# Performance work log

Hardware: AMD Instinct MI355X
Metric: run time of the kernel (lower is better)

## Reference

```python
import jax, jax.numpy as jnp
import numpy as np

B, C_IN, N_IN, N_OUT = 4, 64, 8192, 8192
D1, F, H = 4, 15, 16384  # d+1, filter_size, max_hash_cnt
C_MID, C_OUT = 64, 64
LEAK = 0.01


def setup_inputs() -> dict:
    key = jax.random.key(0)
    ks = jax.random.split(key, 10)
    features = jax.random.normal(ks[0], (B, C_IN, N_IN), jnp.float32)
    in_barycentric = jax.random.uniform(ks[1], (B, D1, N_IN), dtype=jnp.float32)
    # global flat lattice offsets: local vertex id in [0,H) plus per-batch base b*(H+1)
    local_off = jax.random.randint(ks[2], (B, D1, N_IN), 0, H)
    base = (jnp.arange(B, dtype=jnp.int64) * (H + 1))[:, None, None]
    in_lattice_offset = local_off.astype(jnp.int64) + base
    # neighbor ids in [-1, H); -1 means missing -> maps to zero padding slot after +1
    blur_neighbors = (jax.random.randint(ks[3], (B, F, H), 0, H + 1) - 1).astype(jnp.int64)
    out_barycentric = jax.random.uniform(ks[4], (B, D1, N_OUT), dtype=jnp.float32)
    out_lattice_offset = jax.random.randint(ks[5], (B, D1, N_OUT), 0, H).astype(jnp.int64)
    # blur conv params: layer0 Conv2d(C_IN,C_MID,(F,1)) + LeakyReLU, layer1 Conv2d(C_MID,C_OUT,(1,1)) no relu
    W0 = jax.random.normal(ks[6], (C_MID, C_IN, F), jnp.float32) * 0.05
    b0 = jax.random.normal(ks[7], (C_MID,), jnp.float32) * 0.01
    W1 = jax.random.normal(ks[8], (C_OUT, C_MID), jnp.float32) * 0.1
    b1 = jax.random.normal(ks[9], (C_OUT,), jnp.float32) * 0.01
    bias = jnp.zeros((C_OUT,), jnp.float32)  # slice bias, initialized to zeros as in module
    return dict(features=features, in_barycentric=in_barycentric,
                in_lattice_offset=in_lattice_offset, blur_neighbors=blur_neighbors,
                out_barycentric=out_barycentric, out_lattice_offset=out_lattice_offset,
                W0=W0, b0=b0, W1=W1, b1=b1, bias=bias)


def reference(features, in_barycentric, in_lattice_offset, blur_neighbors,
              out_barycentric, out_lattice_offset, W0, b0, W1, b1, bias):
    b_sz, c_in, n_in = features.shape
    max_hash = blur_neighbors.shape[-1]
    # ---- splat: scatter-sum barycentric-weighted features onto lattice vertices ----
    vals = in_barycentric[:, None, :, :] * features[:, :, None, :]      # (B,C,d1,N)
    vals = vals.transpose(0, 2, 3, 1).reshape(-1, c_in)                  # (B*d1*N, C)
    idx = (in_lattice_offset + 1).reshape(-1)                            # (B*d1*N,)
    splat = jax.ops.segment_sum(vals, idx, num_segments=b_sz * (max_hash + 1))
    splat = splat.reshape(b_sz, max_hash + 1, c_in).transpose(0, 2, 1)   # (B,C,H+1)
    # normalization: splat of all-ones feature
    one_splat = jax.ops.segment_sum(in_barycentric.reshape(-1), idx,
                                    num_segments=b_sz * (max_hash + 1))
    one_splat = one_splat.reshape(b_sz, max_hash + 1)
    splat = splat / (one_splat + 1e-5)[:, None, :]
    # ---- blur: gather F neighbors per vertex, then conv over the filter axis ----
    spread = jax.vmap(lambda s, n: s[:, n])(splat, blur_neighbors + 1)   # (B,C,F,H)
    h0 = jnp.einsum('bcfh,ocf->boh', spread, W0) + b0[None, :, None]     # (B,C_mid,H)
    h0 = jnp.where(h0 > 0, h0, LEAK * h0)                                # LeakyReLU
    feat_blurred = jnp.einsum('boh,po->bph', h0, W1) + b1[None, :, None] # (B,C_out,H)
    # ---- slice: barycentric-weighted gather back to output points ----
    tmp = jax.vmap(lambda f, o: f[:, o])(feat_blurred, out_lattice_offset)  # (B,C_out,d1,N_out)
    sliced = (out_barycentric[:, None, :, :] * tmp).sum(axis=2)
    sliced = sliced + bias[None, :, None]
    return sliced
```

## Files before the change

### kernel.cpp

```cpp
#include <hip/hip_runtime.h>

#define NB 4
#define C_IN 64
#define N_IN 8192
#define N_OUT 8192
#define D1 4
#define FS 15
#define HSZ 16384
#define LEAK 0.01f
#define CAP 24
#define POISON 0xAAAAAAAAu

#define NVERT (NB*(HSZ+1))

typedef __attribute__((ext_vector_type(8))) short short8;
typedef __attribute__((ext_vector_type(4))) float floatx4;

#define SPLATB_OFF 0
#define SPLATB_FL  (NVERT*32)
#define W0B_OFF    (SPLATB_OFF + SPLATB_FL)
#define W0B_FL     (64*64*FS/2)
#define W1B_OFF    (W0B_OFF + W0B_FL)
#define W1B_FL     (64*64/2)
#define CNT_OFF    (W1B_OFF + W1B_FL)
#define CNT_FL     (NVERT)
#define BREG_OFF   (CNT_OFF + CNT_FL)
#define FEATB_OFF  (BREG_OFF)
#define FEATB_FL   (NB*N_IN*32)
#define ENTID_OFF  (FEATB_OFF + FEATB_FL)
#define ENT_FL     (NVERT*CAP)
#define ENTW_OFF   (ENTID_OFF + ENT_FL)
#define FB_OFF     (BREG_OFF)

__device__ inline ushort f2bf(float x) {
    uint u = __float_as_uint(x);
    return (ushort)((u + 0x7FFF + ((u >> 16) & 1)) >> 16);
}
__device__ inline float bf2f(ushort b) {
    return __uint_as_float(((uint)b) << 16);
}

__global__ __launch_bounds__(256) void prep(const float* __restrict__ feat,
                                            const float* __restrict__ W0,
                                            const float* __restrict__ W1,
                                            const int* __restrict__ off,
                                            const float* __restrict__ bary,
                                            ushort* __restrict__ featB,
                                            ushort* __restrict__ W0f,
                                            ushort* __restrict__ W1f,
                                            uint* __restrict__ cnt,
                                            int* __restrict__ ent_id,
                                            float* __restrict__ ent_w) {
    __shared__ float t[64 * 65];
    const int blk = blockIdx.x;
    const int tid = threadIdx.x;
    if (blk < 512) {
        const int b  = blk >> 7;
        const int nb = (blk & 127) << 6;
        const int l  = tid & 63;
        const int g  = tid >> 6;
#pragma unroll
        for (int i = 0; i < 16; ++i) {
            int c = g * 16 + i;
            t[c * 65 + l] = feat[((size_t)(b * 64 + c)) * N_IN + nb + l];
        }
        __syncthreads();
#pragma unroll
        for (int i = 0; i < 16; ++i) {
            int n = g * 16 + i;
            featB[((size_t)(b * N_IN) + nb + n) * 64 + l] = f2bf(t[l * 65 + n]);
        }
    } else if (blk < 1024) {
        int e = (blk - 512) * 256 + tid;
        int v = off[e] + 1;
        int n = e & (N_IN - 1);
        int b = e >> 15;
        uint old  = atomicAdd(&cnt[v], 1u);
        uint slot = (old >= POISON) ? (old - POISON) : old;
        if (slot < CAP) {
            ent_id[v * CAP + slot] = b * N_IN + n;
            ent_w [v * CAP + slot] = bary[e];
        }
    } else {
        int e = (blk - 1024) * 256 + tid;
        if (e < 64 * 64 * FS) {
            int j    = e & 7;
            int lane = (e >> 3) & 63;
            int ch   = (e >> 9) & 1;
            int ot   = (e >> 10) & 3;
            int f    = e >> 12;
            int o = ot * 16 + (lane & 15);
            int c = ch * 32 + ((lane >> 4) & 3) * 8 + j;
            W0f[e] = f2bf(W0[(o * 64 + c) * FS + f]);
        } else {
            int e2   = e - 64 * 64 * FS;
            int j    = e2 & 7;
            int lane = (e2 >> 3) & 63;
            int ch   = (e2 >> 9) & 1;
            int pt   = (e2 >> 10) & 3;
            int p = pt * 16 + (lane & 15);
            int o = ch * 32 + ((lane >> 4) & 3) * 8 + j;
            W1f[e2] = f2bf(W1[p * 64 + o]);
        }
    }
}

__global__ __launch_bounds__(256) void gather_splat(const ushort* __restrict__ featB,
                                                    uint* __restrict__ cnt,
                                                    const int* __restrict__ ent_id,
                                                    const float* __restrict__ ent_w,
                                                    ushort* __restrict__ splatB) {
    const int v    = blockIdx.x * 4 + (threadIdx.x >> 6);
    const int lane = threadIdx.x & 63;
    uint cv = cnt[v];
    if (lane == 0) cnt[v] = 0u;
    int c = (int)((cv >= POISON) ? (cv - POISON) : cv);
    if (c > CAP) c = CAP;
    float acc = 0.f, sw = 0.f;
    const int base = v * CAP;
    for (int e0 = 0; e0 < c; e0 += 4) {
        const int kn = c - e0;
        int   id[4];
        float wt[4];
#pragma unroll
        for (int k = 0; k < 4; ++k) {
            id[k] = ent_id[base + e0 + k];
            wt[k] = ent_w [base + e0 + k];
        }
        float fv[4];
#pragma unroll
        for (int k = 0; k < 4; ++k)
            if (k < kn) fv[k] = bf2f(featB[(size_t)id[k] * 64 + lane]);
#pragma unroll
        for (int k = 0; k < 4; ++k)
            if (k < kn) { acc += wt[k] * fv[k]; sw += wt[k]; }
    }
    splatB[(size_t)v * 64 + lane] = f2bf(acc / (sw + 1e-5f));
}

#define XSTR 72
__global__ __launch_bounds__(256, 4) void blur_mfma(const ushort* __restrict__ splatB,
                                                    const int* __restrict__ nbr,
                                                    const ushort* __restrict__ W0f,
                                                    const ushort* __restrict__ W1f,
                                                    const float* __restrict__ b0,
                                                    const float* __restrict__ b1,
                                                    ushort* __restrict__ fb) {
    __shared__ ushort Xs[2][64 * XSTR];

    const int tid = threadIdx.x;
    const int p   = blockIdx.x;
    const int b   = p & 3;
    const int hb  = (p >> 2) << 6;

    const int lane = tid & 63;
    const int w    = tid >> 6;
    const int ow   = w & 1;
    const int hw   = w >> 1;
    const int m    = lane & 15;
    const int q    = lane >> 4;

    const int r    = tid >> 2;
    const int sseg = (tid & 3) << 4;

    const int* nbase = nbr + (b * FS) * HSZ + hb;
    const size_t sbase = (size_t)b * (HSZ + 1) * 64;

    short8 acur[2][2], anxt[2][2];
#pragma unroll
    for (int ot = 0; ot < 2; ++ot)
#pragma unroll
        for (int ch = 0; ch < 2; ++ch)
            acur[ot][ch] = *(const short8*)&W0f[(((ow * 2 + ot) * 2 + ch) * 64 + lane) * 8];

    {
        int v = nbase[r] + 1;
        const ushort* row = splatB + sbase + (size_t)v * 64 + sseg;
        *(short8*)&Xs[0][r * XSTR + sseg]     = *(const short8*)&row[0];
        *(short8*)&Xs[0][r * XSTR + sseg + 8] = *(const short8*)&row[8];
    }
    int nv = nbase[HSZ + r] + 1;
    __syncthreads();

    floatx4 acc[2][2] = {};

    for (int f = 0; f < FS; ++f) {
        const int cur = f & 1, nxt = cur ^ 1;
        short8 px0, px1;
        int nn = 0;
        if (f < FS - 1) {
            const ushort* row = splatB + sbase + (size_t)nv * 64 + sseg;
            px0 = *(const short8*)&row[0];
            px1 = *(const short8*)&row[8];
#pragma unroll
            for (int ot = 0; ot < 2; ++ot)
#pragma unroll
                for (int ch = 0; ch < 2; ++ch)
                    anxt[ot][ch] = *(const short8*)
                        &W0f[((((f + 1) * 4 + ow * 2 + ot) * 2 + ch) * 64 + lane) * 8];
            if (f < FS - 2) nn = nbase[(f + 2) * HSZ + r] + 1;
        }
#pragma unroll
        for (int ch = 0; ch < 2; ++ch) {
            const int ko = ch * 32 + q * 8;
#pragma unroll
            for (int ht = 0; ht < 2; ++ht) {
                short8 bb = *(const short8*)&Xs[cur][(hw * 32 + ht * 16 + m) * XSTR + ko];
                acc[0][ht] = __builtin_amdgcn_mfma_f32_16x16x32_bf16(acur[0][ch], bb, acc[0][ht], 0, 0, 0);
                acc[1][ht] = __builtin_amdgcn_mfma_f32_16x16x32_bf16(acur[1][ch], bb, acc[1][ht], 0, 0, 0);
            }
        }
        if (f < FS - 1) {
            *(short8*)&Xs[nxt][r * XSTR + sseg]     = px0;
            *(short8*)&Xs[nxt][r * XSTR + sseg + 8] = px1;
            nv = nn;
#pragma unroll
            for (int ot = 0; ot < 2; ++ot)
#pragma unroll
                for (int ch = 0; ch < 2; ++ch)
                    acur[ot][ch] = anxt[ot][ch];
        }
        __syncthreads();
    }

    short8 a2[2][2];
#pragma unroll
    for (int pt = 0; pt < 2; ++pt)
#pragma unroll
        for (int ch = 0; ch < 2; ++ch)
            a2[pt][ch] = *(const short8*)&W1f[(((ow * 2 + pt) * 2 + ch) * 64 + lane) * 8];

    ushort* Hs = &Xs[0][0];
#pragma unroll
    for (int ot = 0; ot < 2; ++ot) {
        const float4 b0v = *(const float4*)(b0 + ow * 32 + ot * 16 + q * 4);
#pragma unroll
        for (int ht = 0; ht < 2; ++ht) {
            float v0 = acc[ot][ht][0] + b0v.x; v0 = v0 > 0.f ? v0 : LEAK * v0;
            float v1 = acc[ot][ht][1] + b0v.y; v1 = v1 > 0.f ? v1 : LEAK * v1;
            float v2 = acc[ot][ht][2] + b0v.z; v2 = v2 > 0.f ? v2 : LEAK * v2;
            float v3 = acc[ot][ht][3] + b0v.w; v3 = v3 > 0.f ? v3 : LEAK * v3;
            ushort4 hv;
            hv.x = f2bf(v0); hv.y = f2bf(v1); hv.z = f2bf(v2); hv.w = f2bf(v3);
            *(ushort4*)&Hs[(hw * 32 + ht * 16 + m) * XSTR + ow * 32 + ot * 16 + q * 4] = hv;
        }
    }
    __syncthreads();

    floatx4 acc2[2][2] = {};
#pragma unroll
    for (int ch = 0; ch < 2; ++ch) {
        const int ko = ch * 32 + q * 8;
#pragma unroll
        for (int ht = 0; ht < 2; ++ht) {
            short8 b2 = *(const short8*)&Hs[(hw * 32 + ht * 16 + m) * XSTR + ko];
            acc2[0][ht] = __builtin_amdgcn_mfma_f32_16x16x32_bf16(a2[0][ch], b2, acc2[0][ht], 0, 0, 0);
            acc2[1][ht] = __builtin_amdgcn_mfma_f32_16x16x32_bf16(a2[1][ch], b2, acc2[1][ht], 0, 0, 0);
        }
    }

#pragma unroll
    for (int pt = 0; pt < 2; ++pt) {
        const float4 b1v = *(const float4*)(b1 + ow * 32 + pt * 16 + q * 4);
#pragma unroll
        for (int ht = 0; ht < 2; ++ht) {
            ushort4 ov;
            ov.x = f2bf(acc2[pt][ht][0] + b1v.x);
            ov.y = f2bf(acc2[pt][ht][1] + b1v.y);
            ov.z = f2bf(acc2[pt][ht][2] + b1v.z);
            ov.w = f2bf(acc2[pt][ht][3] + b1v.w);
            *(ushort4*)&fb[((size_t)(b * HSZ) + hb + hw * 32 + ht * 16 + m) * 64
                           + ow * 32 + pt * 16 + q * 4] = ov;
        }
    }
}

__global__ __launch_bounds__(256) void slice_kernel(const ushort* __restrict__ fb,
                                                    const float* __restrict__ ob,
                                                    const int* __restrict__ off,
                                                    const float* __restrict__ bias,
                                                    float* __restrict__ out) {
    __shared__ float tile[64 * 17];
    const int blk  = blockIdx.x;
    const int b    = blk & 3;
    const int nb   = (blk >> 2) << 4;
    const int lane = threadIdx.x & 63;
    const int w    = threadIdx.x >> 6;

    const float bs = bias[lane];
#pragma unroll
    for (int t = 0; t < 4; ++t) {
        int nl = w * 4 + t;
        int n  = nb + nl;
        float acc = bs;
#pragma unroll
        for (int j = 0; j < D1; ++j) {
            float wj = ob[(b * D1 + j) * N_OUT + n];
            int   oj = off[(b * D1 + j) * N_OUT + n];
            acc += wj * bf2f(fb[((size_t)b * HSZ + oj) * 64 + lane]);
        }
        tile[lane * 17 + nl] = acc;
    }
    __syncthreads();
    {
        const int p  = threadIdx.x >> 2;
        const int c4 = (threadIdx.x & 3) << 2;
        float4 v;
        v.x = tile[p * 17 + c4 + 0];
        v.y = tile[p * 17 + c4 + 1];
        v.z = tile[p * 17 + c4 + 2];
        v.w = tile[p * 17 + c4 + 3];
        *(float4*)&out[((size_t)(b * 64 + p)) * N_OUT + nb + c4] = v;
    }
}

extern "C" void kernel_launch(void* const* d_in, const int* in_sizes, int n_in,
                              void* d_out, int out_size, void* d_ws, size_t ws_size,
                              hipStream_t stream) {
    const float* features = (const float*)d_in[0];
    const float* in_bary  = (const float*)d_in[1];
    const int*   in_off   = (const int*)d_in[2];
    const int*   nbr      = (const int*)d_in[3];
    const float* out_bary = (const float*)d_in[4];
    const int*   out_off  = (const int*)d_in[5];
    const float* W0       = (const float*)d_in[6];
    const float* b0       = (const float*)d_in[7];
    const float* W1       = (const float*)d_in[8];
    const float* b1       = (const float*)d_in[9];
    const float* bias     = (const float*)d_in[10];

    float*  ws     = (float*)d_ws;
    ushort* splatB = (ushort*)(ws + SPLATB_OFF);
    ushort* W0f    = (ushort*)(ws + W0B_OFF);
    ushort* W1f    = (ushort*)(ws + W1B_OFF);
    uint*   cnt    = (uint*)(ws + CNT_OFF);
    ushort* featB  = (ushort*)(ws + FEATB_OFF);
    int*    ent_id = (int*)(ws + ENTID_OFF);
    float*  ent_w  = ws + ENTW_OFF;
    ushort* fb     = (ushort*)(ws + FB_OFF);


    prep<<<1280, 256, 0, stream>>>(features, W0, W1, in_off, in_bary,
                                   featB, W0f, W1f, cnt, ent_id, ent_w);
    gather_splat<<<NVERT / 4, 256, 0, stream>>>(featB, cnt, ent_id, ent_w, splatB);
    blur_mfma<<<NB * (HSZ / 64), 256, 0, stream>>>(splatB, nbr, W0f, W1f, b0, b1, fb);
    slice_kernel<<<NB * (N_OUT / 16), 256, 0, stream>>>(fb, out_bary, out_off, bias, (float*)d_out);
}
```

Baseline: 137.4 us.

## Fuse splat, blur and slice stages into one cooperative persistent kernel

Result: slower. 406.3 us (+195.8%).

```diff
diff --git a/kernel.cpp b/kernel.cpp
--- a/kernel.cpp
+++ b/kernel.cpp
@@ -1,4 +1,7 @@
 #include <hip/hip_runtime.h>
+#include <hip/hip_cooperative_groups.h>
+
+namespace cg = cooperative_groups;
 
 #define NB 4
 #define C_IN 64
@@ -32,12 +35,286 @@
 #define ENTW_OFF   (ENTID_OFF + ENT_FL)
 #define FB_OFF     (BREG_OFF)
 
+#define XSTR 72
+
 __device__ inline ushort f2bf(float x) {
     uint u = __float_as_uint(x);
     return (ushort)((u + 0x7FFF + ((u >> 16) & 1)) >> 16);
 }
 __device__ inline float bf2f(ushort b) {
     return __uint_as_float(((uint)b) << 16);
+}
+
+__global__ __launch_bounds__(256, 4) void fused_all(
+    const float* __restrict__ feat, const float* __restrict__ bary,
+    const int* __restrict__ in_off, const int* __restrict__ nbr,
+    const float* __restrict__ ob,   const int* __restrict__ out_off,
+    const float* __restrict__ W0,   const float* __restrict__ b0,
+    const float* __restrict__ W1,   const float* __restrict__ b1,
+    const float* __restrict__ bias,
+    ushort* __restrict__ featB, ushort* __restrict__ W0f, ushort* __restrict__ W1f,
+    uint* cnt, int* __restrict__ ent_id, float* __restrict__ ent_w,
+    ushort* __restrict__ splatB, ushort* __restrict__ fb, float* __restrict__ out)
+{
+    cg::grid_group grid = cg::this_grid();
+    __shared__ __align__(16) ushort sm[2 * 64 * XSTR];
+    const int tid = threadIdx.x;
+    const int nbk = gridDim.x;
+
+    for (int blk = blockIdx.x; blk < 1280; blk += nbk) {
+        if (blk < 512) {
+            float* t = (float*)sm;
+            const int b  = blk >> 7;
+            const int nb = (blk & 127) << 6;
+            const int l  = tid & 63;
+            const int g  = tid >> 6;
+#pragma unroll
+            for (int i = 0; i < 16; ++i) {
+                int c = g * 16 + i;
+                t[c * 65 + l] = feat[((size_t)(b * 64 + c)) * N_IN + nb + l];
+            }
+            __syncthreads();
+#pragma unroll
+            for (int i = 0; i < 16; ++i) {
+                int n = g * 16 + i;
+                featB[((size_t)(b * N_IN) + nb + n) * 64 + l] = f2bf(t[l * 65 + n]);
+            }
+            __syncthreads();
+        } else if (blk < 1024) {
+            int e = (blk - 512) * 256 + tid;
+            int v = in_off[e] + 1;
+            int n = e & (N_IN - 1);
+            int b = e >> 15;
+            uint old  = atomicAdd(&cnt[v], 1u);
+            uint slot = (old >= POISON) ? (old - POISON) : old;
+            if (slot < CAP) {
+                ent_id[v * CAP + slot] = b * N_IN + n;
+                ent_w [v * CAP + slot] = bary[e];
+            }
+        } else {
+            int e = (blk - 1024) * 256 + tid;
+            if (e < 64 * 64 * FS) {
+                int j    = e & 7;
+                int lane = (e >> 3) & 63;
+                int ch   = (e >> 9) & 1;
+                int ot   = (e >> 10) & 3;
+                int f    = e >> 12;
+                int o = ot * 16 + (lane & 15);
+                int c = ch * 32 + ((lane >> 4) & 3) * 8 + j;
+                W0f[e] = f2bf(W0[(o * 64 + c) * FS + f]);
+            } else {
+                int e2   = e - 64 * 64 * FS;
+                int j    = e2 & 7;
+                int lane = (e2 >> 3) & 63;
+                int ch   = (e2 >> 9) & 1;
+                int pt   = (e2 >> 10) & 3;
+                int p = pt * 16 + (lane & 15);
+                int o = ch * 32 + ((lane >> 4) & 3) * 8 + j;
+                W1f[e2] = f2bf(W1[p * 64 + o]);
+            }
+        }
+    }
+    grid.sync();
+
+    {
+        const int lane = tid & 63;
+        for (int vb = blockIdx.x; vb < NVERT / 4; vb += nbk) {
+            const int v = vb * 4 + (tid >> 6);
+            uint cv = cnt[v];
+            if (lane == 0) cnt[v] = 0u;
+            int c = (int)((cv >= POISON) ? (cv - POISON) : cv);
+            if (c > CAP) c = CAP;
+            float acc = 0.f, sw = 0.f;
+            const int base = v * CAP;
+            for (int e0 = 0; e0 < c; e0 += 4) {
+                const int kn = c - e0;
+                int   id[4];
+                float wt[4];
+#pragma unroll
+                for (int k = 0; k < 4; ++k) {
+                    id[k] = ent_id[base + e0 + k];
+                    wt[k] = ent_w [base + e0 + k];
+                }
+                float fv[4];
+#pragma unroll
+                for (int k = 0; k < 4; ++k)
+                    if (k < kn) fv[k] = bf2f(featB[(size_t)id[k] * 64 + lane]);
+#pragma unroll
+                for (int k = 0; k < 4; ++k)
+                    if (k < kn) { acc += wt[k] * fv[k]; sw += wt[k]; }
+            }
+            splatB[(size_t)v * 64 + lane] = f2bf(acc / (sw + 1e-5f));
+        }
+    }
+    grid.sync();
+
+    for (int p = blockIdx.x; p < NB * (HSZ / 64); p += nbk) {
+        ushort* Xs0 = sm;
+        ushort* Xs1 = sm + 64 * XSTR;
+
+        const int b   = p & 3;
+        const int hb  = (p >> 2) << 6;
+
+        const int lane = tid & 63;
+        const int w    = tid >> 6;
+        const int ow   = w & 1;
+        const int hw   = w >> 1;
+        const int m    = lane & 15;
+        const int q    = lane >> 4;
+
+        const int r    = tid >> 2;
+        const int sseg = (tid & 3) << 4;
+
+        const int* nbase = nbr + (b * FS) * HSZ + hb;
+        const size_t sbase = (size_t)b * (HSZ + 1) * 64;
+
+        short8 acur[2][2], anxt[2][2];
+#pragma unroll
+        for (int ot = 0; ot < 2; ++ot)
+#pragma unroll
+            for (int ch = 0; ch < 2; ++ch)
+                acur[ot][ch] = *(const short8*)&W0f[(((ow * 2 + ot) * 2 + ch) * 64 + lane) * 8];
+
+        {
+            int v = nbase[r] + 1;
+            const ushort* row = splatB + sbase + (size_t)v * 64 + sseg;
+            *(short8*)&Xs0[r * XSTR + sseg]     = *(const short8*)&row[0];
+            *(short8*)&Xs0[r * XSTR + sseg + 8] = *(const short8*)&row[8];
+        }
+        int nv = nbase[HSZ + r] + 1;
+        __syncthreads();
+
+        floatx4 acc[2][2] = {};
+
+        for (int f = 0; f < FS; ++f) {
+            ushort* Xc = (f & 1) ? Xs1 : Xs0;
+            ushort* Xn = (f & 1) ? Xs0 : Xs1;
+            short8 px0, px1;
+            int nn = 0;
+            if (f < FS - 1) {
+                const ushort* row = splatB + sbase + (size_t)nv * 64 + sseg;
+                px0 = *(const short8*)&row[0];
+                px1 = *(const short8*)&row[8];
+#pragma unroll
+                for (int ot = 0; ot < 2; ++ot)
+#pragma unroll
+                    for (int ch = 0; ch < 2; ++ch)
+                        anxt[ot][ch] = *(const short8*)
+                            &W0f[((((f + 1) * 4 + ow * 2 + ot) * 2 + ch) * 64 + lane) * 8];
+                if (f < FS - 2) nn = nbase[(f + 2) * HSZ + r] + 1;
+            }
+#pragma unroll
+            for (int ch = 0; ch < 2; ++ch) {
+                const int ko = ch * 32 + q * 8;
+#pragma unroll
+                for (int ht = 0; ht < 2; ++ht) {
+                    short8 bb = *(const short8*)&Xc[(hw * 32 + ht * 16 + m) * XSTR + ko];
+                    acc[0][ht] = __builtin_amdgcn_mfma_f32_16x16x32_bf16(acur[0][ch], bb, acc[0][ht], 0, 0, 0);
+                    acc[1][ht] = __builtin_amdgcn_mfma_f32_16x16x32_bf16(acur[1][ch], bb, acc[1][ht], 0, 0, 0);
+                }
+            }
+            if (f < FS - 1) {
+                *(short8*)&Xn[r * XSTR + sseg]     = px0;
+                *(short8*)&Xn[r * XSTR + sseg + 8] = px1;
+                nv = nn;
+#pragma unroll
+                for (int ot = 0; ot < 2; ++ot)
+#pragma unroll
+                    for (int ch = 0; ch < 2; ++ch)
+                        acur[ot][ch] = anxt[ot][ch];
+            }
+            __syncthreads();
+        }
+
+        short8 a2[2][2];
+#pragma unroll
+        for (int pt = 0; pt < 2; ++pt)
+#pragma unroll
+            for (int ch = 0; ch < 2; ++ch)
+                a2[pt][ch] = *(const short8*)&W1f[(((ow * 2 + pt) * 2 + ch) * 64 + lane) * 8];
+
+        ushort* Hs = Xs0;
+#pragma unroll
+        for (int ot = 0; ot < 2; ++ot) {
+            const float4 b0v = *(const float4*)(b0 + ow * 32 + ot * 16 + q * 4);
+#pragma unroll
+            for (int ht = 0; ht < 2; ++ht) {
+                float v0 = acc[ot][ht][0] + b0v.x; v0 = v0 > 0.f ? v0 : LEAK * v0;
+                float v1 = acc[ot][ht][1] + b0v.y; v1 = v1 > 0.f ? v1 : LEAK * v1;
+                float v2 = acc[ot][ht][2] + b0v.z; v2 = v2 > 0.f ? v2 : LEAK * v2;
+                float v3 = acc[ot][ht][3] + b0v.w; v3 = v3 > 0.f ? v3 : LEAK * v3;
+                ushort4 hv;
+                hv.x = f2bf(v0); hv.y = f2bf(v1); hv.z = f2bf(v2); hv.w = f2bf(v3);
+                *(ushort4*)&Hs[(hw * 32 + ht * 16 + m) * XSTR + ow * 32 + ot * 16 + q * 4] = hv;
+            }
+        }
+        __syncthreads();
+
+        floatx4 acc2[2][2] = {};
+#pragma unroll
+        for (int ch = 0; ch < 2; ++ch) {
+            const int ko = ch * 32 + q * 8;
+#pragma unroll
+            for (int ht = 0; ht < 2; ++ht) {
+                short8 b2 = *(const short8*)&Hs[(hw * 32 + ht * 16 + m) * XSTR + ko];
+                acc2[0][ht] = __builtin_amdgcn_mfma_f32_16x16x32_bf16(a2[0][ch], b2, acc2[0][ht], 0, 0, 0);
+                acc2[1][ht] = __builtin_amdgcn_mfma_f32_16x16x32_bf16(a2[1][ch], b2, acc2[1][ht], 0, 0, 0);
+            }
+        }
+
+#pragma unroll
+        for (int pt = 0; pt < 2; ++pt) {
+            const float4 b1v = *(const float4*)(b1 + ow * 32 + pt * 16 + q * 4);
+#pragma unroll
+            for (int ht = 0; ht < 2; ++ht) {
+                ushort4 ov;
+                ov.x = f2bf(acc2[pt][ht][0] + b1v.x);
+                ov.y = f2bf(acc2[pt][ht][1] + b1v.y);
+                ov.z = f2bf(acc2[pt][ht][2] + b1v.z);
+                ov.w = f2bf(acc2[pt][ht][3] + b1v.w);
+                *(ushort4*)&fb[((size_t)(b * HSZ) + hb + hw * 32 + ht * 16 + m) * 64
+                               + ow * 32 + pt * 16 + q * 4] = ov;
+            }
+        }
+        __syncthreads();
+    }
+    grid.sync();
+
+    {
+        float* tile = (float*)sm;
+        const int lane = tid & 63;
+        const int w    = tid >> 6;
+        const float bs = bias[lane];
+        for (int vb = blockIdx.x; vb < NB * (N_OUT / 16); vb += nbk) {
+            const int b  = vb & 3;
+            const int nb = (vb >> 2) << 4;
+#pragma unroll
+            for (int t = 0; t < 4; ++t) {
+                int nl = w * 4 + t;
+                int n  = nb + nl;
+                float acc = bs;
+#pragma unroll
+                for (int j = 0; j < D1; ++j) {
+                    float wj = ob[(b * D1 + j) * N_OUT + n];
+                    int   oj = out_off[(b * D1 + j) * N_OUT + n];
+                    acc += wj * bf2f(fb[((size_t)b * HSZ + oj) * 64 + lane]);
+                }
+                tile[lane * 17 + nl] = acc;
+            }
+            __syncthreads();
+            {
+                const int pp = tid >> 2;
+                const int c4 = (tid & 3) << 2;
+                float4 v;
+                v.x = tile[pp * 17 + c4 + 0];
+                v.y = tile[pp * 17 + c4 + 1];
+                v.z = tile[pp * 17 + c4 + 2];
+                v.w = tile[pp * 17 + c4 + 3];
+                *(float4*)&out[((size_t)(b * 64 + pp)) * N_OUT + nb + c4] = v;
+            }
+            __syncthreads();
+        }
+    }
 }
 
 __global__ __launch_bounds__(256) void prep(const float* __restrict__ feat,
@@ -138,7 +415,6 @@
     splatB[(size_t)v * 64 + lane] = f2bf(acc / (sw + 1e-5f));
 }
 
-#define XSTR 72
 __global__ __launch_bounds__(256, 4) void blur_mfma(const ushort* __restrict__ splatB,
                                                     const int* __restrict__ nbr,
                                                     const ushort* __restrict__ W0f,
@@ -338,11 +614,38 @@
     int*    ent_id = (int*)(ws + ENTID_OFF);
     float*  ent_w  = ws + ENTW_OFF;
     ushort* fb     = (ushort*)(ws + FB_OFF);
-
-
-    prep<<<1280, 256, 0, stream>>>(features, W0, W1, in_off, in_bary,
-                                   featB, W0f, W1f, cnt, ent_id, ent_w);
-    gather_splat<<<NVERT / 4, 256, 0, stream>>>(featB, cnt, ent_id, ent_w, splatB);
-    blur_mfma<<<NB * (HSZ / 64), 256, 0, stream>>>(splatB, nbr, W0f, W1f, b0, b1, fb);
-    slice_kernel<<<NB * (N_OUT / 16), 256, 0, stream>>>(fb, out_bary, out_off, bias, (float*)d_out);
-}
+    float*  outp   = (float*)d_out;
+
+    static int grid = 0;
+    if (grid == 0) {
+        int dev = 0;
+        (void)hipGetDevice(&dev);
+        hipDeviceProp_t prop;
+        int cus = 256;
+        if (hipGetDeviceProperties(&prop, dev) == hipSuccess && prop.multiProcessorCount > 0)
+            cus = prop.multiProcessorCount;
+        int nb = 0;
+        if (hipOccupancyMaxActiveBlocksPerMultiprocessor(&nb, fused_all, 256, 0) != hipSuccess || nb < 1)
+            nb = 1;
+        long g = (long)cus * nb;
+        grid = (int)(g > 1024 ? 1024 : (g < 8 ? 8 : g));
+    }
+
+    void* kargs[] = {
+        (void*)&features, (void*)&in_bary, (void*)&in_off, (void*)&nbr,
+        (void*)&out_bary, (void*)&out_off,
+        (void*)&W0, (void*)&b0, (void*)&W1, (void*)&b1, (void*)&bias,
+        (void*)&featB, (void*)&W0f, (void*)&W1f, (void*)&cnt,
+        (void*)&ent_id, (void*)&ent_w, (void*)&splatB, (void*)&fb, (void*)&outp
+    };
+    hipError_t err = hipLaunchCooperativeKernel((const void*)fused_all,
+                                                dim3(grid), dim3(256),
+                                                kargs, 0, stream);
+    if (err != hipSuccess) {
+        prep<<<1280, 256, 0, stream>>>(features, W0, W1, in_off, in_bary,
+                                       featB, W0f, W1f, cnt, ent_id, ent_w);
+        gather_splat<<<NVERT / 4, 256, 0, stream>>>(featB, cnt, ent_id, ent_w, splatB);
+        blur_mfma<<<NB * (HSZ / 64), 256, 0, stream>>>(splatB, nbr, W0f, W1f, b0, b1, fb);
+        slice_kernel<<<NB * (N_OUT / 16), 256, 0, stream>>>(fb, out_bary, out_off, bias, outp);
+    }
+}
```
